# Kernel optimization log

Measured on AMD Instinct MI355X. Metric: run time of the kernel, lower is better.

The kernel has to match this reference:

```python
import jax, jax.numpy as jnp
import numpy as np

N, D = 4096, 32


def setup_inputs() -> dict:
    key = jax.random.key(0)
    k1, _ = jax.random.split(key)
    particles = jax.random.normal(k1, (N, D), dtype=jnp.float32)
    length_scale = jnp.ones((1,), dtype=jnp.float32)
    return {"particles": particles, "length_scale": length_scale}


def reference(particles, length_scale):
    # SVGDModel.calculate_gradient with an RBF kernel and standard-Gaussian density.
    num_particles = particles.shape[0]
    ls2 = length_scale[0] ** 2

    # pairwise differences: diff[i, j] = x_i - x_j  -> [N, N, D]
    diff = particles[:, None, :] - particles[None, :, :]
    sq_dists = jnp.sum(diff * diff, axis=-1)               # [N, N]

    # gram_matrix = k(x_i, x_j) = exp(-||x_i - x_j||^2 / (2 l^2))
    gram_matrix = jnp.exp(-sq_dists / (2.0 * ls2))          # [N, N]

    # density.score for standard Gaussian: grad log p(x) = -x
    score_matrix = -particles                               # [N, D]

    # kernel_gradient[i, j] = grad_{x_i} k(x_i, x_j) = -(x_i - x_j)/l^2 * k
    kernel_gradient = -(diff / ls2) * gram_matrix[..., None]  # [N, N, D]

    kernel_score_term = jnp.einsum('ij,jk->ik', gram_matrix, score_matrix)  # [N, D]
    kernel_gradient_term = jnp.sum(kernel_gradient, axis=0)                 # [N, D]

    phi = (kernel_score_term + kernel_gradient_term) / num_particles
    return phi
```

## Files before the change

kernel.cpp:

```cpp
#include <hip/hip_runtime.h>

#define NPART 4096
#define DIM 32
#define LOG2E 1.44269504088896340736f
#define SHSTR 36

typedef _Float16 f16x8 __attribute__((ext_vector_type(8)));
typedef _Float16 f16x4 __attribute__((ext_vector_type(4)));
typedef float f32x4 __attribute__((ext_vector_type(4)));

__global__ __launch_bounds__(256, 4) void svgd_onepass_kernel(
    const float* __restrict__ X, const float* __restrict__ ls,
    float* __restrict__ out) {
  __shared__ __align__(16) unsigned char smem[16896];
  _Float16* sHi = (_Float16*)smem;
  _Float16* sLo = (_Float16*)(smem + 4608);
  _Float16* sXT = (_Float16*)(smem + 9216);
  float* sM2 = (float*)(smem + 13824);
  float* sT = (float*)smem;
  float* sS = (float*)(smem + 16384);

  const int tid = threadIdx.x;
  const int lane = tid & 63;
  const int g = lane >> 4;
  const int li = lane & 15;
  const int wave = tid >> 6;
  const int i0 = blockIdx.x * 32;
  const int jb0 = blockIdx.y * 512;

  const float lsv = ls[0];
  const float inv = 1.f / (lsv * lsv);
  const float si2 = LOG2E * inv;
  const float hm = 0.5f * si2;

  const float4* X4 = (const float4*)X;

  f16x8 bh0, bl0, bh1, bl1;
  float mi0, mi1;
  {
    const int r0 = i0 + li, r1 = i0 + 16 + li;
    float4 a0 = X4[(size_t)r0 * 8 + g], b0 = X4[(size_t)r0 * 8 + 4 + g];
    float4 a1 = X4[(size_t)r1 * 8 + g], b1 = X4[(size_t)r1 * 8 + 4 + g];
    float t0[8] = {a0.x, a0.y, a0.z, a0.w, b0.x, b0.y, b0.z, b0.w};
    float t1[8] = {a1.x, a1.y, a1.z, a1.w, b1.x, b1.y, b1.z, b1.w};
    float n0 = 0.f, n1 = 0.f;
#pragma unroll
    for (int e = 0; e < 8; ++e) {
      n0 = fmaf(t0[e], t0[e], n0);
      n1 = fmaf(t1[e], t1[e], n1);
      _Float16 h0 = (_Float16)t0[e];
      _Float16 h1 = (_Float16)t1[e];
      bh0[e] = h0; bl0[e] = (_Float16)(t0[e] - (float)h0);
      bh1[e] = h1; bl1[e] = (_Float16)(t1[e] - (float)h1);
    }
    n0 += __shfl_xor(n0, 16, 64);
    n0 += __shfl_xor(n0, 32, 64);
    n1 += __shfl_xor(n1, 16, 64);
    n1 += __shfl_xor(n1, 32, 64);
    mi0 = n0 * hm;
    mi1 = n1 * hm;
  }

  f32x4 c2a0 = {0.f, 0.f, 0.f, 0.f}, c2b0 = {0.f, 0.f, 0.f, 0.f};
  f32x4 c2a1 = {0.f, 0.f, 0.f, 0.f}, c2b1 = {0.f, 0.f, 0.f, 0.f};
  float Sp0 = 0.f, Sp1 = 0.f;

  for (int s = 0; s < 8; ++s) {
    __syncthreads();
    {
      const int r = tid >> 2, ss = tid & 3;
      const int row = jb0 + s * 64 + r;
      float4 a = X4[(size_t)row * 8 + ss];
      float4 b = X4[(size_t)row * 8 + 4 + ss];
      float tv[8] = {a.x, a.y, a.z, a.w, b.x, b.y, b.z, b.w};
      _Float16 h[8];
      f16x4 pl0, pl1;
      float nrm = 0.f;
#pragma unroll
      for (int e = 0; e < 8; ++e) {
        nrm = fmaf(tv[e], tv[e], nrm);
        _Float16 hh = (_Float16)tv[e];
        h[e] = hh;
        _Float16 ll = (_Float16)(tv[e] - (float)hh);
        if (e < 4) pl0[e] = ll; else pl1[e - 4] = ll;
      }
      f16x4 ph0 = {h[0], h[1], h[2], h[3]};
      f16x4 ph1 = {h[4], h[5], h[6], h[7]};
      *(f16x4*)(sHi + r * SHSTR + ss * 8) = ph0;
      *(f16x4*)(sHi + r * SHSTR + ss * 8 + 4) = ph1;
      *(f16x4*)(sLo + r * SHSTR + ss * 8) = pl0;
      *(f16x4*)(sLo + r * SHSTR + ss * 8 + 4) = pl1;
#pragma unroll
      for (int e = 0; e < 8; ++e) {
        const int d = (e < 4) ? (4 * ss + e) : (16 + 4 * ss + (e - 4));
        sXT[d * 72 + r] = h[e];
      }
      nrm += __shfl_xor(nrm, 1, 64);
      nrm += __shfl_xor(nrm, 2, 64);
      if (ss == 0) sM2[r] = nrm * hm;
    }
    __syncthreads();

    {
      const int jloc = wave * 16;
      const _Float16* hb = sHi + (jloc + li) * SHSTR + g * 8;
      const _Float16* lb = sLo + (jloc + li) * SHSTR + g * 8;
      f16x4 AhL = *(const f16x4*)(hb);
      f16x4 AhH = *(const f16x4*)(hb + 4);
      f16x4 AlL = *(const f16x4*)(lb);
      f16x4 AlH = *(const f16x4*)(lb + 4);
      f16x8 Ah = __builtin_shufflevector(AhL, AhH, 0, 1, 2, 3, 4, 5, 6, 7);
      f16x8 Al = __builtin_shufflevector(AlL, AlH, 0, 1, 2, 3, 4, 5, 6, 7);
      f16x4 Ba = *(const f16x4*)(sXT + li * 72 + jloc + 4 * g);
      f16x4 Bb = *(const f16x4*)(sXT + (16 + li) * 72 + jloc + 4 * g);
      f32x4 Mj = *(const f32x4*)(sM2 + jloc + 4 * g);

      f32x4 c10 = {0.f, 0.f, 0.f, 0.f}, c11 = {0.f, 0.f, 0.f, 0.f};
      c10 = __builtin_amdgcn_mfma_f32_16x16x32_f16(Ah, bh0, c10, 0, 0, 0);
      c11 = __builtin_amdgcn_mfma_f32_16x16x32_f16(Ah, bh1, c11, 0, 0, 0);
      c10 = __builtin_amdgcn_mfma_f32_16x16x32_f16(Al, bh0, c10, 0, 0, 0);
      c11 = __builtin_amdgcn_mfma_f32_16x16x32_f16(Al, bh1, c11, 0, 0, 0);
      c10 = __builtin_amdgcn_mfma_f32_16x16x32_f16(Ah, bl0, c10, 0, 0, 0);
      c11 = __builtin_amdgcn_mfma_f32_16x16x32_f16(Ah, bl1, c11, 0, 0, 0);
      f16x4 a20, a21;
#pragma unroll
      for (int r = 0; r < 4; ++r) {
        float k0 = exp2f(fmaf(c10[r], si2, -(mi0 + Mj[r])));
        float k1 = exp2f(fmaf(c11[r], si2, -(mi1 + Mj[r])));
        Sp0 += k0;
        Sp1 += k1;
        a20[r] = (_Float16)k0;
        a21[r] = (_Float16)k1;
      }
      c2a0 = __builtin_amdgcn_mfma_f32_16x16x16f16(a20, Ba, c2a0, 0, 0, 0);
      c2b0 = __builtin_amdgcn_mfma_f32_16x16x16f16(a20, Bb, c2b0, 0, 0, 0);
      c2a1 = __builtin_amdgcn_mfma_f32_16x16x16f16(a21, Ba, c2a1, 0, 0, 0);
      c2b1 = __builtin_amdgcn_mfma_f32_16x16x16f16(a21, Bb, c2b1, 0, 0, 0);
    }
  }

  __syncthreads();

#pragma unroll
  for (int r = 0; r < 4; ++r) {
    sT[(wave * 32 + 4 * g + r) * 32 + li] = c2a0[r];
    sT[(wave * 32 + 4 * g + r) * 32 + 16 + li] = c2b0[r];
    sT[(wave * 32 + 16 + 4 * g + r) * 32 + li] = c2a1[r];
    sT[(wave * 32 + 16 + 4 * g + r) * 32 + 16 + li] = c2b1[r];
  }
  {
    float s0 = Sp0, s1 = Sp1;
    s0 += __shfl_xor(s0, 16, 64);
    s0 += __shfl_xor(s0, 32, 64);
    s1 += __shfl_xor(s1, 16, 64);
    s1 += __shfl_xor(s1, 32, 64);
    if (g == 0) {
      sS[wave * 32 + li] = s0;
      sS[wave * 32 + 16 + li] = s1;
    }
  }
  __syncthreads();

  const float c1f = inv * (1.f / NPART);
  const float c2f = (1.f + inv) * (1.f / NPART);
#pragma unroll
  for (int q = 0; q < 4; ++q) {
    const int v = q * 256 + tid;
    const int row = v >> 5, d = v & 31;
    const float T = sT[(0 * 32 + row) * 32 + d] + sT[(1 * 32 + row) * 32 + d] +
                    sT[(2 * 32 + row) * 32 + d] + sT[(3 * 32 + row) * 32 + d];
    const float S = sS[0 * 32 + row] + sS[1 * 32 + row] + sS[2 * 32 + row] +
                    sS[3 * 32 + row];
    const size_t idx = (size_t)(i0 + row) * DIM + d;
    unsafeAtomicAdd(&out[idx], c1f * S * X[idx] - c2f * T);
  }
}

#define TJ 64
__global__ __launch_bounds__(256) void svgd_direct_kernel(const float* __restrict__ X,
                                                          const float* __restrict__ ls,
                                                          float* __restrict__ out) {
  __shared__ float4 sX[TJ * 8];
  const int tid = threadIdx.x;
  const int row = blockIdx.x * 256 + tid;
  const float lsv = ls[0];
  const float ls2 = lsv * lsv;
  const float inv2 = 0.5f / ls2;
  float4 xi[8];
  const float4* xr = reinterpret_cast<const float4*>(X + (size_t)row * DIM);
#pragma unroll
  for (int q = 0; q < 8; ++q) xi[q] = xr[q];
  float4 acc[8];
#pragma unroll
  for (int q = 0; q < 8; ++q) acc[q] = make_float4(0.f, 0.f, 0.f, 0.f);
  float S = 0.f;
  for (int jb = 0; jb < NPART; jb += TJ) {
    __syncthreads();
    const float4* src = reinterpret_cast<const float4*>(X + (size_t)jb * DIM);
    for (int t = tid; t < TJ * 8; t += 256) sX[t] = src[t];
    __syncthreads();
    for (int t = 0; t < TJ; ++t) {
      const float4* xj = &sX[t * 8];
      float4 v[8];
      float d0 = 0.f, d1 = 0.f, d2 = 0.f, d3 = 0.f;
#pragma unroll
      for (int q = 0; q < 8; ++q) {
        v[q] = xj[q];
        float ax = xi[q].x - v[q].x; d0 = fmaf(ax, ax, d0);
        float ay = xi[q].y - v[q].y; d1 = fmaf(ay, ay, d1);
        float az = xi[q].z - v[q].z; d2 = fmaf(az, az, d2);
        float aw = xi[q].w - v[q].w; d3 = fmaf(aw, aw, d3);
      }
      float k = __expf(-((d0 + d1) + (d2 + d3)) * inv2);
      S += k;
#pragma unroll
      for (int q = 0; q < 8; ++q) {
        acc[q].x = fmaf(k, v[q].x, acc[q].x);
        acc[q].y = fmaf(k, v[q].y, acc[q].y);
        acc[q].z = fmaf(k, v[q].z, acc[q].z);
        acc[q].w = fmaf(k, v[q].w, acc[q].w);
      }
    }
  }
  const float inv = 1.f / ls2;
  const float c1 = inv * S;
  const float c2 = 1.f + inv;
  float4* o = reinterpret_cast<float4*>(out + (size_t)row * DIM);
#pragma unroll
  for (int q = 0; q < 8; ++q) {
    float4 r;
    r.x = (c1 * xi[q].x - c2 * acc[q].x) * (1.f / NPART);
    r.y = (c1 * xi[q].y - c2 * acc[q].y) * (1.f / NPART);
    r.z = (c1 * xi[q].z - c2 * acc[q].z) * (1.f / NPART);
    r.w = (c1 * xi[q].w - c2 * acc[q].w) * (1.f / NPART);
    o[q] = r;
  }
}

extern "C" void kernel_launch(void* const* d_in, const int* in_sizes, int n_in,
                              void* d_out, int out_size, void* d_ws, size_t ws_size,
                              hipStream_t stream) {
  const float* X = (const float*)d_in[0];
  const float* ls = (const float*)d_in[1];
  float* out = (float*)d_out;
  (void)d_ws;
  (void)ws_size;

  hipError_t e =
      hipMemsetAsync(d_out, 0, (size_t)out_size * sizeof(float), stream);
  if (e == hipSuccess) {
    dim3 grid(NPART / 32, 8);
    svgd_onepass_kernel<<<grid, 256, 0, stream>>>(X, ls, out);
    return;
  }
  svgd_direct_kernel<<<NPART / 256, 256, 0, stream>>>(X, ls, out);
}
```

Before: 25.65 us.

## Double-buffer staged particle tiles and merge hi/lo/transposed layouts into one buffer

Stages each 64-row tile of particles into one of two shared-memory buffers, so the next tile is loaded and split while the current one is computed, with one barrier per step instead of two. It also merges the hi, lo and transposed-hi arrays into one interleaved row layout, where each row holds hi and lo halves of 16 halves per group. The transposed B operand is now gathered with strided scalar LDS reads instead of a separate transposed copy. The cost is more shared memory, possible bank conflicts on the gathers, and more registers from the full unroll.

```diff
diff --git a/kernel.cpp b/kernel.cpp
--- a/kernel.cpp
+++ b/kernel.cpp
@@ -3,7 +3,7 @@
 #define NPART 4096
 #define DIM 32
 #define LOG2E 1.44269504088896340736f
-#define SHSTR 36
+#define RSTR 72
 
 typedef _Float16 f16x8 __attribute__((ext_vector_type(8)));
 typedef _Float16 f16x4 __attribute__((ext_vector_type(4)));
@@ -12,13 +12,13 @@
 __global__ __launch_bounds__(256, 4) void svgd_onepass_kernel(
     const float* __restrict__ X, const float* __restrict__ ls,
     float* __restrict__ out) {
-  __shared__ __align__(16) unsigned char smem[16896];
-  _Float16* sHi = (_Float16*)smem;
-  _Float16* sLo = (_Float16*)(smem + 4608);
-  _Float16* sXT = (_Float16*)(smem + 9216);
-  float* sM2 = (float*)(smem + 13824);
+  __shared__ __align__(16) unsigned char smem[19456];
+  _Float16* hl0 = (_Float16*)smem;
+  float* m0 = (float*)(smem + 9216);
+  _Float16* hl1 = (_Float16*)(smem + 9472);
+  float* m1 = (float*)(smem + 18688);
+  float* sS = (float*)(smem + 18944);
   float* sT = (float*)smem;
-  float* sS = (float*)(smem + 16384);
 
   const int tid = threadIdx.x;
   const int lane = tid & 63;
@@ -65,81 +65,77 @@
   f32x4 c2a1 = {0.f, 0.f, 0.f, 0.f}, c2b1 = {0.f, 0.f, 0.f, 0.f};
   float Sp0 = 0.f, Sp1 = 0.f;
 
+  const int r_st = tid >> 2, ss_st = tid & 3;
+
+  auto STAGE = [&](int s, _Float16* hl, float* m2b) {
+    const int row = jb0 + s * 64 + r_st;
+    float4 a = X4[(size_t)row * 8 + ss_st];
+    float4 b = X4[(size_t)row * 8 + 4 + ss_st];
+    float tv[8] = {a.x, a.y, a.z, a.w, b.x, b.y, b.z, b.w};
+    f16x8 hi, lo;
+    float nrm = 0.f;
+#pragma unroll
+    for (int e = 0; e < 8; ++e) {
+      nrm = fmaf(tv[e], tv[e], nrm);
+      _Float16 hh = (_Float16)tv[e];
+      hi[e] = hh;
+      lo[e] = (_Float16)(tv[e] - (float)hh);
+    }
+    _Float16* cell = hl + r_st * RSTR + ss_st * 16;
+    *(f16x8*)(cell) = hi;
+    *(f16x8*)(cell + 8) = lo;
+    nrm += __shfl_xor(nrm, 1, 64);
+    nrm += __shfl_xor(nrm, 2, 64);
+    if (ss_st == 0) m2b[r_st] = nrm * hm;
+  };
+
+  auto COMP = [&](const _Float16* hl, const float* m2b) {
+    const int jloc = wave * 16;
+    const _Float16* cell = hl + (jloc + li) * RSTR + g * 16;
+    f16x8 Ah = *(const f16x8*)(cell);
+    f16x8 Al = *(const f16x8*)(cell + 8);
+    const _Float16* bb = hl + (jloc + 4 * g) * RSTR + (li >> 2) * 16 + (li & 3);
+    f16x4 Ba, Bb;
+#pragma unroll
+    for (int e = 0; e < 4; ++e) {
+      Ba[e] = bb[e * RSTR];
+      Bb[e] = bb[e * RSTR + 4];
+    }
+    f32x4 Mj = *(const f32x4*)(m2b + jloc + 4 * g);
+
+    f32x4 c10 = {0.f, 0.f, 0.f, 0.f}, c11 = {0.f, 0.f, 0.f, 0.f};
+    c10 = __builtin_amdgcn_mfma_f32_16x16x32_f16(Ah, bh0, c10, 0, 0, 0);
+    c11 = __builtin_amdgcn_mfma_f32_16x16x32_f16(Ah, bh1, c11, 0, 0, 0);
+    c10 = __builtin_amdgcn_mfma_f32_16x16x32_f16(Al, bh0, c10, 0, 0, 0);
+    c11 = __builtin_amdgcn_mfma_f32_16x16x32_f16(Al, bh1, c11, 0, 0, 0);
+    c10 = __builtin_amdgcn_mfma_f32_16x16x32_f16(Ah, bl0, c10, 0, 0, 0);
+    c11 = __builtin_amdgcn_mfma_f32_16x16x32_f16(Ah, bl1, c11, 0, 0, 0);
+    f16x4 a20, a21;
+#pragma unroll
+    for (int r = 0; r < 4; ++r) {
+      float k0 = exp2f(fmaf(c10[r], si2, -(mi0 + Mj[r])));
+      float k1 = exp2f(fmaf(c11[r], si2, -(mi1 + Mj[r])));
+      Sp0 += k0;
+      Sp1 += k1;
+      a20[r] = (_Float16)k0;
+      a21[r] = (_Float16)k1;
+    }
+    c2a0 = __builtin_amdgcn_mfma_f32_16x16x16f16(a20, Ba, c2a0, 0, 0, 0);
+    c2b0 = __builtin_amdgcn_mfma_f32_16x16x16f16(a20, Bb, c2b0, 0, 0, 0);
+    c2a1 = __builtin_amdgcn_mfma_f32_16x16x16f16(a21, Ba, c2a1, 0, 0, 0);
+    c2b1 = __builtin_amdgcn_mfma_f32_16x16x16f16(a21, Bb, c2b1, 0, 0, 0);
+  };
+
+  STAGE(0, hl0, m0);
+  __syncthreads();
+#pragma unroll
   for (int s = 0; s < 8; ++s) {
+    _Float16* curH = (s & 1) ? hl1 : hl0;
+    float* curM = (s & 1) ? m1 : m0;
+    if (s < 7) STAGE(s + 1, (s & 1) ? hl0 : hl1, (s & 1) ? m0 : m1);
+    COMP(curH, curM);
     __syncthreads();
-    {
-      const int r = tid >> 2, ss = tid & 3;
-      const int row = jb0 + s * 64 + r;
-      float4 a = X4[(size_t)row * 8 + ss];
-      float4 b = X4[(size_t)row * 8 + 4 + ss];
-      float tv[8] = {a.x, a.y, a.z, a.w, b.x, b.y, b.z, b.w};
-      _Float16 h[8];
-      f16x4 pl0, pl1;
-      float nrm = 0.f;
-#pragma unroll
-      for (int e = 0; e < 8; ++e) {
-        nrm = fmaf(tv[e], tv[e], nrm);
-        _Float16 hh = (_Float16)tv[e];
-        h[e] = hh;
-        _Float16 ll = (_Float16)(tv[e] - (float)hh);
-        if (e < 4) pl0[e] = ll; else pl1[e - 4] = ll;
-      }
-      f16x4 ph0 = {h[0], h[1], h[2], h[3]};
-      f16x4 ph1 = {h[4], h[5], h[6], h[7]};
-      *(f16x4*)(sHi + r * SHSTR + ss * 8) = ph0;
-      *(f16x4*)(sHi + r * SHSTR + ss * 8 + 4) = ph1;
-      *(f16x4*)(sLo + r * SHSTR + ss * 8) = pl0;
-      *(f16x4*)(sLo + r * SHSTR + ss * 8 + 4) = pl1;
-#pragma unroll
-      for (int e = 0; e < 8; ++e) {
-        const int d = (e < 4) ? (4 * ss + e) : (16 + 4 * ss + (e - 4));
-        sXT[d * 72 + r] = h[e];
-      }
-      nrm += __shfl_xor(nrm, 1, 64);
-      nrm += __shfl_xor(nrm, 2, 64);
-      if (ss == 0) sM2[r] = nrm * hm;
-    }
-    __syncthreads();
-
-    {
-      const int jloc = wave * 16;
-      const _Float16* hb = sHi + (jloc + li) * SHSTR + g * 8;
-      const _Float16* lb = sLo + (jloc + li) * SHSTR + g * 8;
-      f16x4 AhL = *(const f16x4*)(hb);
-      f16x4 AhH = *(const f16x4*)(hb + 4);
-      f16x4 AlL = *(const f16x4*)(lb);
-      f16x4 AlH = *(const f16x4*)(lb + 4);
-      f16x8 Ah = __builtin_shufflevector(AhL, AhH, 0, 1, 2, 3, 4, 5, 6, 7);
-      f16x8 Al = __builtin_shufflevector(AlL, AlH, 0, 1, 2, 3, 4, 5, 6, 7);
-      f16x4 Ba = *(const f16x4*)(sXT + li * 72 + jloc + 4 * g);
-      f16x4 Bb = *(const f16x4*)(sXT + (16 + li) * 72 + jloc + 4 * g);
-      f32x4 Mj = *(const f32x4*)(sM2 + jloc + 4 * g);
-
-      f32x4 c10 = {0.f, 0.f, 0.f, 0.f}, c11 = {0.f, 0.f, 0.f, 0.f};
-      c10 = __builtin_amdgcn_mfma_f32_16x16x32_f16(Ah, bh0, c10, 0, 0, 0);
-      c11 = __builtin_amdgcn_mfma_f32_16x16x32_f16(Ah, bh1, c11, 0, 0, 0);
-      c10 = __builtin_amdgcn_mfma_f32_16x16x32_f16(Al, bh0, c10, 0, 0, 0);
-      c11 = __builtin_amdgcn_mfma_f32_16x16x32_f16(Al, bh1, c11, 0, 0, 0);
-      c10 = __builtin_amdgcn_mfma_f32_16x16x32_f16(Ah, bl0, c10, 0, 0, 0);
-      c11 = __builtin_amdgcn_mfma_f32_16x16x32_f16(Ah, bl1, c11, 0, 0, 0);
-      f16x4 a20, a21;
-#pragma unroll
-      for (int r = 0; r < 4; ++r) {
-        float k0 = exp2f(fmaf(c10[r], si2, -(mi0 + Mj[r])));
-        float k1 = exp2f(fmaf(c11[r], si2, -(mi1 + Mj[r])));
-        Sp0 += k0;
-        Sp1 += k1;
-        a20[r] = (_Float16)k0;
-        a21[r] = (_Float16)k1;
-      }
-      c2a0 = __builtin_amdgcn_mfma_f32_16x16x16f16(a20, Ba, c2a0, 0, 0, 0);
-      c2b0 = __builtin_amdgcn_mfma_f32_16x16x16f16(a20, Bb, c2b0, 0, 0, 0);
-      c2a1 = __builtin_amdgcn_mfma_f32_16x16x16f16(a21, Ba, c2a1, 0, 0, 0);
-      c2b1 = __builtin_amdgcn_mfma_f32_16x16x16f16(a21, Bb, c2b1, 0, 0, 0);
-    }
-  }
-
-  __syncthreads();
+  }
 
 #pragma unroll
   for (int r = 0; r < 4; ++r) {
```

After: 25.82 us. About the same (+0.7%).
